# Performance work log

Measured on AMD Instinct MI355X. Metric: run time of the kernel, lower is better.

Reference implementation:

```python
import jax, jax.numpy as jnp
import numpy as np

NUM_NODES = 10000
NUM_EDGES = 320000
FEAT_DIM = 256


def setup_inputs() -> dict:
    key = jax.random.key(0)
    k1, k2 = jax.random.split(key)
    msg = jax.random.normal(k1, (NUM_EDGES, FEAT_DIM), dtype=jnp.float32)
    edge_index = jax.random.randint(k2, (2, NUM_EDGES), 0, NUM_NODES, dtype=jnp.int64)
    return {"msg": msg, "edge_index": edge_index}


def reference(msg, edge_index):
    # Faithful math of one_hot(target).T @ msg == segment-sum of msg over target nodes.
    target_nodes = edge_index[1]
    agg = jax.ops.segment_sum(msg, target_nodes, num_segments=NUM_NODES)  # [num_nodes, feat_dim]
    return agg
```

## Files before the change

kernel.cpp:

```cpp
#include <hip/hip_runtime.h>

#define NUM_NODES 10000
#define NUM_EDGES 320000
#define FEAT_DIM  256
#define OVF_CAP   4096

typedef float  f32x4 __attribute__((ext_vector_type(4)));


__global__ __launch_bounds__(256) void fill_buckets(
    const int* __restrict__ tgt,
    int*       __restrict__ cursor,
    int*       __restrict__ buckets,
    int        cap,
    int*       __restrict__ ovf_cnt,
    int*       __restrict__ ovf)
{
    int base = (blockIdx.x * blockDim.x + threadIdx.x) * 4;
    if (base >= NUM_EDGES) return;
    int4 t4 = *(const int4*)(tgt + base);
    int ts[4] = {t4.x, t4.y, t4.z, t4.w};
    #pragma unroll
    for (int k = 0; k < 4; ++k) {
        int e = base + k;
        int t = ts[k];
        int idx = atomicAdd(&cursor[t], 1);
        if (idx < cap) {
            buckets[(size_t)t * cap + idx] = e;
        } else {
            int o = atomicAdd(ovf_cnt, 1);
            if (o < OVF_CAP) { ovf[2 * o] = e; ovf[2 * o + 1] = t; }
        }
    }
}

__device__ __forceinline__ f32x4 nt_load4(const f32x4* p) {
    return __builtin_nontemporal_load(p);
}

__global__ __launch_bounds__(256) void gather_sum(
    const f32x4* __restrict__ msg4,
    const int*   __restrict__ cursor,
    const int*   __restrict__ buckets,
    f32x4*       __restrict__ out4,
    int          cap)
{
    int g    = threadIdx.x >> 6;
    int lane = threadIdx.x & 63;
    int n    = blockIdx.x * 4 + g;
    if (n >= NUM_NODES) return;

    int deg = cursor[n];
    if (deg > cap) deg = cap;
    const int* bl = buckets + (size_t)n * cap;

    f32x4 acc = (f32x4)(0.f);

    int m1  = deg < 64 ? deg : 64;
    int e_l = (lane < m1) ? bl[lane] : 0;
    int i = 0;
    for (; i + 8 <= m1; i += 8) {
        int e0 = __shfl(e_l, i),     e1 = __shfl(e_l, i + 1);
        int e2 = __shfl(e_l, i + 2), e3 = __shfl(e_l, i + 3);
        int e4 = __shfl(e_l, i + 4), e5 = __shfl(e_l, i + 5);
        int e6 = __shfl(e_l, i + 6), e7 = __shfl(e_l, i + 7);
        f32x4 v0 = nt_load4(msg4 + (size_t)e0 * 64 + lane);
        f32x4 v1 = nt_load4(msg4 + (size_t)e1 * 64 + lane);
        f32x4 v2 = nt_load4(msg4 + (size_t)e2 * 64 + lane);
        f32x4 v3 = nt_load4(msg4 + (size_t)e3 * 64 + lane);
        f32x4 v4 = nt_load4(msg4 + (size_t)e4 * 64 + lane);
        f32x4 v5 = nt_load4(msg4 + (size_t)e5 * 64 + lane);
        f32x4 v6 = nt_load4(msg4 + (size_t)e6 * 64 + lane);
        f32x4 v7 = nt_load4(msg4 + (size_t)e7 * 64 + lane);
        acc += ((v0 + v1) + (v2 + v3)) + ((v4 + v5) + (v6 + v7));
    }
    for (; i + 4 <= m1; i += 4) {
        int e0 = __shfl(e_l, i),     e1 = __shfl(e_l, i + 1);
        int e2 = __shfl(e_l, i + 2), e3 = __shfl(e_l, i + 3);
        f32x4 v0 = nt_load4(msg4 + (size_t)e0 * 64 + lane);
        f32x4 v1 = nt_load4(msg4 + (size_t)e1 * 64 + lane);
        f32x4 v2 = nt_load4(msg4 + (size_t)e2 * 64 + lane);
        f32x4 v3 = nt_load4(msg4 + (size_t)e3 * 64 + lane);
        acc += (v0 + v1) + (v2 + v3);
    }
    for (; i < m1; ++i) {
        int e = __shfl(e_l, i);
        acc += nt_load4(msg4 + (size_t)e * 64 + lane);
    }

    if (deg > 64) {
        int m2   = deg - 64;
        int e_l2 = (lane < m2) ? bl[64 + lane] : 0;
        for (int j = 0; j < m2; ++j) {
            int e = __shfl(e_l2, j);
            acc += nt_load4(msg4 + (size_t)e * 64 + lane);
        }
    }

    __builtin_nontemporal_store(acc, out4 + (size_t)n * 64 + lane);
}

__global__ __launch_bounds__(256) void ovf_cleanup(
    const float* __restrict__ msg,
    float*       __restrict__ out,
    const int*   __restrict__ ovf_cnt,
    const int*   __restrict__ ovf)
{
    int cnt = *ovf_cnt;
    if (cnt > OVF_CAP) cnt = OVF_CAP;
    for (int o = blockIdx.x; o < cnt; o += gridDim.x) {
        int e = ovf[2 * o], t = ovf[2 * o + 1];
        const float* m  = msg + (size_t)e * FEAT_DIM;
        float*       op = out + (size_t)t * FEAT_DIM;
        for (int f = threadIdx.x; f < FEAT_DIM; f += blockDim.x)
            atomicAdd(op + f, m[f]);
    }
}

__global__ __launch_bounds__(256) void scatter_add_kernel(
    const float4* __restrict__ msg4,
    const int*    __restrict__ tgt,
    float*        __restrict__ out)
{
    int idx = blockIdx.x * blockDim.x + threadIdx.x;
    int e  = idx >> 6;
    int f4 = idx & 63;
    if (e >= NUM_EDGES) return;
    float4 v = msg4[(size_t)e * 64 + f4];
    int t = tgt[e];
    float* o = out + (size_t)t * FEAT_DIM + f4 * 4;
    atomicAdd(o + 0, v.x);
    atomicAdd(o + 1, v.y);
    atomicAdd(o + 2, v.z);
    atomicAdd(o + 3, v.w);
}

extern "C" void kernel_launch(void* const* d_in, const int* in_sizes, int n_in,
                              void* d_out, int out_size, void* d_ws, size_t ws_size,
                              hipStream_t stream) {
    const float*  msg   = (const float*)d_in[0];
    const f32x4*  msg4  = (const f32x4*)d_in[0];
    const int*    eidx  = (const int*)d_in[1];
    const int*    tgt   = eidx + NUM_EDGES;
    float*        out   = (float*)d_out;

    const size_t header = ((size_t)NUM_NODES + 1 + 2 * OVF_CAP) * sizeof(int);

    int cap = 0;
    if (ws_size > header) {
        size_t avail = (ws_size - header) / ((size_t)NUM_NODES * sizeof(int));
        cap = avail >= 128 ? 128 : (avail >= 64 ? 64 : 0);
    }

    if (cap > 0) {
        int* cursor  = (int*)d_ws;
        int* ovf_cnt = cursor + NUM_NODES;
        int* ovf     = ovf_cnt + 1;
        int* buckets = ovf + 2 * OVF_CAP;

        (void)hipMemsetAsync(cursor, 0, ((size_t)NUM_NODES + 1) * sizeof(int), stream);

        fill_buckets<<<(NUM_EDGES / 4 + 255) / 256, 256, 0, stream>>>(
            tgt, cursor, buckets, cap, ovf_cnt, ovf);
        gather_sum<<<NUM_NODES / 4, 256, 0, stream>>>(
            msg4, cursor, buckets, (f32x4*)out, cap);
        ovf_cleanup<<<8, 256, 0, stream>>>(msg, out, ovf_cnt, ovf);
    } else {
        (void)hipMemsetAsync(out, 0, (size_t)out_size * sizeof(float), stream);
        const int total = NUM_EDGES * 64;
        scatter_add_kernel<<<(total + 255) / 256, 256, 0, stream>>>((const float4*)d_in[0], tgt, out);
    }
}
```

Before: 95.76 us.

## Fuse bucket fill, gather and overflow cleanup into one cooperative kernel

Replaces the memset plus three separate kernel launches with a single cooperative persistent kernel of 1024 blocks. Grid-wide syncs separate the cursor zeroing, bucket filling, gather-sum and overflow cleanup phases. The aim is to remove launch overhead and inter-kernel gaps. In exchange it adds grid.sync costs, caps parallelism at the resident grid size, and falls back to the old path if the cooperative launch fails.

After: 371.4 us. +287.9%, slower.

```diff
diff --git a/kernel.cpp b/kernel.cpp
--- a/kernel.cpp
+++ b/kernel.cpp
@@ -1,55 +1,29 @@
 #include <hip/hip_runtime.h>
+#include <hip/hip_cooperative_groups.h>
+
+namespace cg = cooperative_groups;
 
 #define NUM_NODES 10000
 #define NUM_EDGES 320000
 #define FEAT_DIM  256
 #define OVF_CAP   4096
-
-typedef float  f32x4 __attribute__((ext_vector_type(4)));
-
-
-__global__ __launch_bounds__(256) void fill_buckets(
-    const int* __restrict__ tgt,
-    int*       __restrict__ cursor,
-    int*       __restrict__ buckets,
-    int        cap,
-    int*       __restrict__ ovf_cnt,
-    int*       __restrict__ ovf)
-{
-    int base = (blockIdx.x * blockDim.x + threadIdx.x) * 4;
-    if (base >= NUM_EDGES) return;
-    int4 t4 = *(const int4*)(tgt + base);
-    int ts[4] = {t4.x, t4.y, t4.z, t4.w};
-    #pragma unroll
-    for (int k = 0; k < 4; ++k) {
-        int e = base + k;
-        int t = ts[k];
-        int idx = atomicAdd(&cursor[t], 1);
-        if (idx < cap) {
-            buckets[(size_t)t * cap + idx] = e;
-        } else {
-            int o = atomicAdd(ovf_cnt, 1);
-            if (o < OVF_CAP) { ovf[2 * o] = e; ovf[2 * o + 1] = t; }
-        }
-    }
-}
+#define GRID_BLKS 1024
+#define BLOCK     256
+
+typedef float f32x4 __attribute__((ext_vector_type(4)));
+
 
 __device__ __forceinline__ f32x4 nt_load4(const f32x4* p) {
     return __builtin_nontemporal_load(p);
 }
 
-__global__ __launch_bounds__(256) void gather_sum(
+__device__ __forceinline__ void gather_node(
     const f32x4* __restrict__ msg4,
     const int*   __restrict__ cursor,
     const int*   __restrict__ buckets,
     f32x4*       __restrict__ out4,
-    int          cap)
-{
-    int g    = threadIdx.x >> 6;
-    int lane = threadIdx.x & 63;
-    int n    = blockIdx.x * 4 + g;
-    if (n >= NUM_NODES) return;
-
+    int cap, int n, int lane)
+{
     int deg = cursor[n];
     if (deg > cap) deg = cap;
     const int* bl = buckets + (size_t)n * cap;
@@ -87,7 +61,6 @@
         int e = __shfl(e_l, i);
         acc += nt_load4(msg4 + (size_t)e * 64 + lane);
     }
-
     if (deg > 64) {
         int m2   = deg - 64;
         int e_l2 = (lane < m2) ? bl[64 + lane] : 0;
@@ -100,11 +73,99 @@
     __builtin_nontemporal_store(acc, out4 + (size_t)n * 64 + lane);
 }
 
+__global__ __launch_bounds__(BLOCK, 4) void fused_all(
+    const f32x4* __restrict__ msg4,
+    const float* __restrict__ msg,
+    const int*   __restrict__ tgt,
+    int*         __restrict__ cursor,
+    int*         __restrict__ buckets,
+    int          cap,
+    int*         __restrict__ ovf_cnt,
+    int*         __restrict__ ovf,
+    f32x4*       __restrict__ out4,
+    float*       __restrict__ out)
+{
+    cg::grid_group grid = cg::this_grid();
+    const int tid = blockIdx.x * BLOCK + threadIdx.x;
+
+    for (int i = tid; i < NUM_NODES + 1; i += GRID_BLKS * BLOCK) cursor[i] = 0;
+    grid.sync();
+
+    for (int base = tid * 4; base < NUM_EDGES; base += GRID_BLKS * BLOCK * 4) {
+        int4 t4 = *(const int4*)(tgt + base);
+        int ts[4] = {t4.x, t4.y, t4.z, t4.w};
+        #pragma unroll
+        for (int k = 0; k < 4; ++k) {
+            int e = base + k;
+            int t = ts[k];
+            int idx = atomicAdd(&cursor[t], 1);
+            if (idx < cap) {
+                buckets[(size_t)t * cap + idx] = e;
+            } else {
+                int o = atomicAdd(ovf_cnt, 1);
+                if (o < OVF_CAP) { ovf[2 * o] = e; ovf[2 * o + 1] = t; }
+            }
+        }
+    }
+    grid.sync();
+
+    {
+        int g    = threadIdx.x >> 6;
+        int lane = threadIdx.x & 63;
+        for (int n = blockIdx.x * 4 + g; n < NUM_NODES; n += GRID_BLKS * 4)
+            gather_node(msg4, cursor, buckets, out4, cap, n, lane);
+    }
+    grid.sync();
+
+    {
+        int cnt = *ovf_cnt;
+        if (cnt > OVF_CAP) cnt = OVF_CAP;
+        for (int o = blockIdx.x; o < cnt; o += GRID_BLKS) {
+            int e = ovf[2 * o], t = ovf[2 * o + 1];
+            const float* m  = msg + (size_t)e * FEAT_DIM;
+            float*       op = out + (size_t)t * FEAT_DIM;
+            for (int f = threadIdx.x; f < FEAT_DIM; f += BLOCK)
+                atomicAdd(op + f, m[f]);
+        }
+    }
+}
+
+__global__ __launch_bounds__(256) void fill_buckets(
+    const int* __restrict__ tgt, int* __restrict__ cursor, int* __restrict__ buckets,
+    int cap, int* __restrict__ ovf_cnt, int* __restrict__ ovf)
+{
+    int base = (blockIdx.x * blockDim.x + threadIdx.x) * 4;
+    if (base >= NUM_EDGES) return;
+    int4 t4 = *(const int4*)(tgt + base);
+    int ts[4] = {t4.x, t4.y, t4.z, t4.w};
+    #pragma unroll
+    for (int k = 0; k < 4; ++k) {
+        int e = base + k;
+        int t = ts[k];
+        int idx = atomicAdd(&cursor[t], 1);
+        if (idx < cap) {
+            buckets[(size_t)t * cap + idx] = e;
+        } else {
+            int o = atomicAdd(ovf_cnt, 1);
+            if (o < OVF_CAP) { ovf[2 * o] = e; ovf[2 * o + 1] = t; }
+        }
+    }
+}
+
+__global__ __launch_bounds__(256) void gather_sum(
+    const f32x4* __restrict__ msg4, const int* __restrict__ cursor,
+    const int* __restrict__ buckets, f32x4* __restrict__ out4, int cap)
+{
+    int g    = threadIdx.x >> 6;
+    int lane = threadIdx.x & 63;
+    int n    = blockIdx.x * 4 + g;
+    if (n >= NUM_NODES) return;
+    gather_node(msg4, cursor, buckets, out4, cap, n, lane);
+}
+
 __global__ __launch_bounds__(256) void ovf_cleanup(
-    const float* __restrict__ msg,
-    float*       __restrict__ out,
-    const int*   __restrict__ ovf_cnt,
-    const int*   __restrict__ ovf)
+    const float* __restrict__ msg, float* __restrict__ out,
+    const int* __restrict__ ovf_cnt, const int* __restrict__ ovf)
 {
     int cnt = *ovf_cnt;
     if (cnt > OVF_CAP) cnt = OVF_CAP;
@@ -118,9 +179,7 @@
 }
 
 __global__ __launch_bounds__(256) void scatter_add_kernel(
-    const float4* __restrict__ msg4,
-    const int*    __restrict__ tgt,
-    float*        __restrict__ out)
+    const float4* __restrict__ msg4, const int* __restrict__ tgt, float* __restrict__ out)
 {
     int idx = blockIdx.x * blockDim.x + threadIdx.x;
     int e  = idx >> 6;
@@ -138,11 +197,11 @@
 extern "C" void kernel_launch(void* const* d_in, const int* in_sizes, int n_in,
                               void* d_out, int out_size, void* d_ws, size_t ws_size,
                               hipStream_t stream) {
-    const float*  msg   = (const float*)d_in[0];
-    const f32x4*  msg4  = (const f32x4*)d_in[0];
-    const int*    eidx  = (const int*)d_in[1];
-    const int*    tgt   = eidx + NUM_EDGES;
-    float*        out   = (float*)d_out;
+    const float* msg  = (const float*)d_in[0];
+    const f32x4* msg4 = (const f32x4*)d_in[0];
+    const int*   eidx = (const int*)d_in[1];
+    const int*   tgt  = eidx + NUM_EDGES;
+    float*       out  = (float*)d_out;
 
     const size_t header = ((size_t)NUM_NODES + 1 + 2 * OVF_CAP) * sizeof(int);
 
@@ -157,17 +216,26 @@
         int* ovf_cnt = cursor + NUM_NODES;
         int* ovf     = ovf_cnt + 1;
         int* buckets = ovf + 2 * OVF_CAP;
-
-        (void)hipMemsetAsync(cursor, 0, ((size_t)NUM_NODES + 1) * sizeof(int), stream);
-
-        fill_buckets<<<(NUM_EDGES / 4 + 255) / 256, 256, 0, stream>>>(
-            tgt, cursor, buckets, cap, ovf_cnt, ovf);
-        gather_sum<<<NUM_NODES / 4, 256, 0, stream>>>(
-            msg4, cursor, buckets, (f32x4*)out, cap);
-        ovf_cleanup<<<8, 256, 0, stream>>>(msg, out, ovf_cnt, ovf);
+        f32x4* out4  = (f32x4*)out;
+
+        void* args[] = { (void*)&msg4, (void*)&msg, (void*)&tgt,
+                         (void*)&cursor, (void*)&buckets, (void*)&cap,
+                         (void*)&ovf_cnt, (void*)&ovf, (void*)&out4, (void*)&out };
+        hipError_t err = hipLaunchCooperativeKernel(
+            (const void*)fused_all, dim3(GRID_BLKS), dim3(BLOCK), args, 0, stream);
+
+        if (err != hipSuccess) {
+            (void)hipMemsetAsync(cursor, 0, ((size_t)NUM_NODES + 1) * sizeof(int), stream);
+            fill_buckets<<<(NUM_EDGES / 4 + 255) / 256, 256, 0, stream>>>(
+                tgt, cursor, buckets, cap, ovf_cnt, ovf);
+            gather_sum<<<NUM_NODES / 4, 256, 0, stream>>>(
+                msg4, cursor, buckets, out4, cap);
+            ovf_cleanup<<<8, 256, 0, stream>>>(msg, out, ovf_cnt, ovf);
+        }
     } else {
         (void)hipMemsetAsync(out, 0, (size_t)out_size * sizeof(float), stream);
         const int total = NUM_EDGES * 64;
-        scatter_add_kernel<<<(total + 255) / 256, 256, 0, stream>>>((const float4*)d_in[0], tgt, out);
-    }
-}
+        scatter_add_kernel<<<(total + 255) / 256, 256, 0, stream>>>(
+            (const float4*)d_in[0], tgt, out);
+    }
+}
```

## Fix bucket capacity at 64, fold overflow handling into gather, drop cleanup kernel

Applied to the files above, without the earlier changes.

Hard-codes the bucket capacity to a compile-time constant of 64 instead of choosing 128 or 64 from workspace size. Overflow edges are now summed inside gather_sum by each overflowing node scanning the overflow list, which removes the separate ovf_cleanup launch and its atomics. The message loads also switch from nontemporal to ordinary cached loads. Nodes with degree above 64 must linearly scan the whole overflow list, which can cost a lot if many nodes overflow. The overflow buffer is also smaller than the previous 128-slot buckets would have needed, so edges beyond it may be dropped.

Result: no change. 94.18 us (-1.6%).

```diff
diff --git a/kernel.cpp b/kernel.cpp
--- a/kernel.cpp
+++ b/kernel.cpp
@@ -3,16 +3,16 @@
 #define NUM_NODES 10000
 #define NUM_EDGES 320000
 #define FEAT_DIM  256
+#define CAP       64
 #define OVF_CAP   4096
 
-typedef float  f32x4 __attribute__((ext_vector_type(4)));
+typedef float f32x4 __attribute__((ext_vector_type(4)));
 
 
 __global__ __launch_bounds__(256) void fill_buckets(
     const int* __restrict__ tgt,
     int*       __restrict__ cursor,
     int*       __restrict__ buckets,
-    int        cap,
     int*       __restrict__ ovf_cnt,
     int*       __restrict__ ovf)
 {
@@ -25,8 +25,8 @@
         int e = base + k;
         int t = ts[k];
         int idx = atomicAdd(&cursor[t], 1);
-        if (idx < cap) {
-            buckets[(size_t)t * cap + idx] = e;
+        if (idx < CAP) {
+            buckets[t * CAP + idx] = e;
         } else {
             int o = atomicAdd(ovf_cnt, 1);
             if (o < OVF_CAP) { ovf[2 * o] = e; ovf[2 * o + 1] = t; }
@@ -34,29 +34,25 @@
     }
 }
 
-__device__ __forceinline__ f32x4 nt_load4(const f32x4* p) {
-    return __builtin_nontemporal_load(p);
-}
-
 __global__ __launch_bounds__(256) void gather_sum(
     const f32x4* __restrict__ msg4,
     const int*   __restrict__ cursor,
     const int*   __restrict__ buckets,
-    f32x4*       __restrict__ out4,
-    int          cap)
+    const int*   __restrict__ ovf_cnt,
+    const int*   __restrict__ ovf,
+    f32x4*       __restrict__ out4)
 {
     int g    = threadIdx.x >> 6;
     int lane = threadIdx.x & 63;
     int n    = blockIdx.x * 4 + g;
     if (n >= NUM_NODES) return;
 
-    int deg = cursor[n];
-    if (deg > cap) deg = cap;
-    const int* bl = buckets + (size_t)n * cap;
+    int deg  = cursor[n];
+    int m1   = deg < CAP ? deg : CAP;
+    const int* bl = buckets + n * CAP;
 
     f32x4 acc = (f32x4)(0.f);
 
-    int m1  = deg < 64 ? deg : 64;
     int e_l = (lane < m1) ? bl[lane] : 0;
     int i = 0;
     for (; i + 8 <= m1; i += 8) {
@@ -64,63 +60,46 @@
         int e2 = __shfl(e_l, i + 2), e3 = __shfl(e_l, i + 3);
         int e4 = __shfl(e_l, i + 4), e5 = __shfl(e_l, i + 5);
         int e6 = __shfl(e_l, i + 6), e7 = __shfl(e_l, i + 7);
-        f32x4 v0 = nt_load4(msg4 + (size_t)e0 * 64 + lane);
-        f32x4 v1 = nt_load4(msg4 + (size_t)e1 * 64 + lane);
-        f32x4 v2 = nt_load4(msg4 + (size_t)e2 * 64 + lane);
-        f32x4 v3 = nt_load4(msg4 + (size_t)e3 * 64 + lane);
-        f32x4 v4 = nt_load4(msg4 + (size_t)e4 * 64 + lane);
-        f32x4 v5 = nt_load4(msg4 + (size_t)e5 * 64 + lane);
-        f32x4 v6 = nt_load4(msg4 + (size_t)e6 * 64 + lane);
-        f32x4 v7 = nt_load4(msg4 + (size_t)e7 * 64 + lane);
+        f32x4 v0 = msg4[(size_t)e0 * 64 + lane];
+        f32x4 v1 = msg4[(size_t)e1 * 64 + lane];
+        f32x4 v2 = msg4[(size_t)e2 * 64 + lane];
+        f32x4 v3 = msg4[(size_t)e3 * 64 + lane];
+        f32x4 v4 = msg4[(size_t)e4 * 64 + lane];
+        f32x4 v5 = msg4[(size_t)e5 * 64 + lane];
+        f32x4 v6 = msg4[(size_t)e6 * 64 + lane];
+        f32x4 v7 = msg4[(size_t)e7 * 64 + lane];
         acc += ((v0 + v1) + (v2 + v3)) + ((v4 + v5) + (v6 + v7));
     }
     for (; i + 4 <= m1; i += 4) {
         int e0 = __shfl(e_l, i),     e1 = __shfl(e_l, i + 1);
         int e2 = __shfl(e_l, i + 2), e3 = __shfl(e_l, i + 3);
-        f32x4 v0 = nt_load4(msg4 + (size_t)e0 * 64 + lane);
-        f32x4 v1 = nt_load4(msg4 + (size_t)e1 * 64 + lane);
-        f32x4 v2 = nt_load4(msg4 + (size_t)e2 * 64 + lane);
-        f32x4 v3 = nt_load4(msg4 + (size_t)e3 * 64 + lane);
+        f32x4 v0 = msg4[(size_t)e0 * 64 + lane];
+        f32x4 v1 = msg4[(size_t)e1 * 64 + lane];
+        f32x4 v2 = msg4[(size_t)e2 * 64 + lane];
+        f32x4 v3 = msg4[(size_t)e3 * 64 + lane];
         acc += (v0 + v1) + (v2 + v3);
     }
     for (; i < m1; ++i) {
         int e = __shfl(e_l, i);
-        acc += nt_load4(msg4 + (size_t)e * 64 + lane);
+        acc += msg4[(size_t)e * 64 + lane];
     }
 
-    if (deg > 64) {
-        int m2   = deg - 64;
-        int e_l2 = (lane < m2) ? bl[64 + lane] : 0;
-        for (int j = 0; j < m2; ++j) {
-            int e = __shfl(e_l2, j);
-            acc += nt_load4(msg4 + (size_t)e * 64 + lane);
+    if (deg > CAP) {
+        int cnt = *ovf_cnt;
+        if (cnt > OVF_CAP) cnt = OVF_CAP;
+        for (int o = 0; o < cnt; ++o) {
+            if (ovf[2 * o + 1] == n) {
+                int e = ovf[2 * o];
+                acc += msg4[(size_t)e * 64 + lane];
+            }
         }
     }
 
     __builtin_nontemporal_store(acc, out4 + (size_t)n * 64 + lane);
 }
 
-__global__ __launch_bounds__(256) void ovf_cleanup(
-    const float* __restrict__ msg,
-    float*       __restrict__ out,
-    const int*   __restrict__ ovf_cnt,
-    const int*   __restrict__ ovf)
-{
-    int cnt = *ovf_cnt;
-    if (cnt > OVF_CAP) cnt = OVF_CAP;
-    for (int o = blockIdx.x; o < cnt; o += gridDim.x) {
-        int e = ovf[2 * o], t = ovf[2 * o + 1];
-        const float* m  = msg + (size_t)e * FEAT_DIM;
-        float*       op = out + (size_t)t * FEAT_DIM;
-        for (int f = threadIdx.x; f < FEAT_DIM; f += blockDim.x)
-            atomicAdd(op + f, m[f]);
-    }
-}
-
 __global__ __launch_bounds__(256) void scatter_add_kernel(
-    const float4* __restrict__ msg4,
-    const int*    __restrict__ tgt,
-    float*        __restrict__ out)
+    const float4* __restrict__ msg4, const int* __restrict__ tgt, float* __restrict__ out)
 {
     int idx = blockIdx.x * blockDim.x + threadIdx.x;
     int e  = idx >> 6;
@@ -138,21 +117,15 @@
 extern "C" void kernel_launch(void* const* d_in, const int* in_sizes, int n_in,
                               void* d_out, int out_size, void* d_ws, size_t ws_size,
                               hipStream_t stream) {
-    const float*  msg   = (const float*)d_in[0];
-    const f32x4*  msg4  = (const f32x4*)d_in[0];
-    const int*    eidx  = (const int*)d_in[1];
-    const int*    tgt   = eidx + NUM_EDGES;
-    float*        out   = (float*)d_out;
+    const f32x4* msg4 = (const f32x4*)d_in[0];
+    const int*   eidx = (const int*)d_in[1];
+    const int*   tgt  = eidx + NUM_EDGES;
+    float*       out  = (float*)d_out;
 
-    const size_t header = ((size_t)NUM_NODES + 1 + 2 * OVF_CAP) * sizeof(int);
+    const size_t need = ((size_t)NUM_NODES + 1 + 2 * OVF_CAP
+                         + (size_t)NUM_NODES * CAP) * sizeof(int);
 
-    int cap = 0;
-    if (ws_size > header) {
-        size_t avail = (ws_size - header) / ((size_t)NUM_NODES * sizeof(int));
-        cap = avail >= 128 ? 128 : (avail >= 64 ? 64 : 0);
-    }
-
-    if (cap > 0) {
+    if (ws_size >= need) {
         int* cursor  = (int*)d_ws;
         int* ovf_cnt = cursor + NUM_NODES;
         int* ovf     = ovf_cnt + 1;
@@ -161,13 +134,13 @@
         (void)hipMemsetAsync(cursor, 0, ((size_t)NUM_NODES + 1) * sizeof(int), stream);
 
         fill_buckets<<<(NUM_EDGES / 4 + 255) / 256, 256, 0, stream>>>(
-            tgt, cursor, buckets, cap, ovf_cnt, ovf);
+            tgt, cursor, buckets, ovf_cnt, ovf);
         gather_sum<<<NUM_NODES / 4, 256, 0, stream>>>(
-            msg4, cursor, buckets, (f32x4*)out, cap);
-        ovf_cleanup<<<8, 256, 0, stream>>>(msg, out, ovf_cnt, ovf);
+            msg4, cursor, buckets, ovf_cnt, ovf, (f32x4*)out);
     } else {
         (void)hipMemsetAsync(out, 0, (size_t)out_size * sizeof(float), stream);
         const int total = NUM_EDGES * 64;
-        scatter_add_kernel<<<(total + 255) / 256, 256, 0, stream>>>((const float4*)d_in[0], tgt, out);
+        scatter_add_kernel<<<(total + 255) / 256, 256, 0, stream>>>(
+            (const float4*)d_in[0], tgt, out);
     }
 }
```
